# Kernel tuning notes

Measured on AMD Instinct MI355X. Metric: run time of the kernel, lower is better.

## Reference

```python
import jax, jax.numpy as jnp
import numpy as np
from jax import lax


def _nextpow2(v):
    return int(np.ceil(np.log2(abs(v))))


def _dct_matrix(N):
    # Orthonormal DCT-II matrix C: dct(x, norm='ortho') along last axis == x @ C.T
    # C is orthogonal, so idct(y, norm='ortho') == y @ C.
    n = jnp.arange(N, dtype=jnp.float32)
    k = n[:, None]
    C = 2.0 * jnp.cos(jnp.pi * (2.0 * n[None, :] + 1.0) * k / (2.0 * N))
    s = jnp.where(jnp.arange(N) == 0,
                  1.0 / jnp.sqrt(4.0 * N),
                  1.0 / jnp.sqrt(2.0 * N)).astype(jnp.float32)
    return s[:, None] * C


def setup_inputs() -> dict:
    key = jax.random.key(0)
    x = jax.random.normal(key, (2, 1, 128, 128), dtype=jnp.float32)
    tau = jnp.asarray(7.7e-11, dtype=jnp.float32)
    chi = jnp.asarray(0.03, dtype=jnp.float32)
    return {"x": x, "tau": tau, "chi": chi}


def _forward(x, c0=1.0, sigma=1.0):
    B, _, Nz, Nx = x.shape
    Lx = 2 ** (_nextpow2(2 * Nx) + 1)  # padded width (512 for Nx=128)
    Ly = 2 ** (_nextpow2(2 * Nz) + 1)  # padded height (512 for Nz=128)
    Cy = _dct_matrix(Ly)
    Cx = Cy if Lx == Ly else _dct_matrix(Lx)

    # np.block([[Z, W, ZP_col], [Z, Z, ZP_col], [ZP_row]]) places W at rows 0:Nz, cols Nx:2Nx
    P = jnp.zeros((B, Ly, Lx), x.dtype).at[:, 0:Nz, Nx:2 * Nx].set(x[:, 0])

    # 2D orthonormal DCT-II: P_hat = Cy @ P @ Cx.T
    P_hat = jnp.einsum('ki,bij,lj->bkl', Cy, P, Cx)

    # Only row 0 of the 2D IDCT is kept per timestep; row-0 of the axis-0 IDCT is
    # a fixed weighted sum with weights a[k] = Cy[k, 0].
    a = Cy[:, 0]
    M = a[None, :, None] * P_hat  # (B, Ly, Lx)

    kx = jnp.arange(Lx, dtype=jnp.float32) / Lx * jnp.pi
    ky = jnp.arange(Ly, dtype=jnp.float32) / Ly * jnp.pi
    F = jnp.sqrt(ky[:, None] ** 2 + kx[None, :] ** 2)  # f.T in the source: (Ly, Lx)

    def step(carry, t):
        phase = jnp.cos(c0 * F * t)                 # (Ly, Lx), shared over batch
        return carry, jnp.einsum('kj,bkj->bj', phase, M)

    _, V = lax.scan(step, None, jnp.arange(Ly, dtype=jnp.float32))  # (T, B, Lx)

    # Remaining IDCT along the last axis, then /3
    Pdet = jnp.transpose(V @ Cx, (1, 0, 2)) / 3.0   # (B, T=Ly, Lx)

    # additive noise: N(0, sigma * std(Pdet)) per batch element (np.std -> ddof=0)
    std = jnp.std(Pdet, axis=(1, 2), keepdims=True)
    noise = jax.random.normal(jax.random.key(42), Pdet.shape, Pdet.dtype) * (sigma * std)
    return (Pdet + noise)[:, None]                  # (B, 1, Ly, Lx)


def reference(x, tau, chi):
    # tau, chi are module parameters but unused in the original forward path
    return _forward(x)
```

## Files before the change

### kernel.cpp

```cpp
#include <hip/hip_runtime.h>
#include <stdint.h>
#include <math.h>


#define HALF_N 262144
#define PI_F 3.14159274101257324f


__device__ __forceinline__ uint32_t rotl32(uint32_t v, int r) {
  return (v << r) | (v >> (32 - r));
}

__device__ __forceinline__ float erfinv_xla(float x) {
  float w = -log1pf(__fmul_rn(-x, x));
  float p;
  if (w < 5.0f) {
    w = w - 2.5f;
    p = 2.81022636e-08f;
    p = fmaf(p, w, 3.43273939e-07f);
    p = fmaf(p, w, -3.5233877e-06f);
    p = fmaf(p, w, -4.39150654e-06f);
    p = fmaf(p, w, 0.00021858087f);
    p = fmaf(p, w, -0.00125372503f);
    p = fmaf(p, w, -0.00417768164f);
    p = fmaf(p, w, 0.246640727f);
    p = fmaf(p, w, 1.50140941f);
  } else {
    w = __fsqrt_rn(w) - 3.0f;
    p = -0.000200214257f;
    p = fmaf(p, w, 0.000100950558f);
    p = fmaf(p, w, 0.00134934322f);
    p = fmaf(p, w, -0.00367342844f);
    p = fmaf(p, w, 0.00573950773f);
    p = fmaf(p, w, -0.0076224613f);
    p = fmaf(p, w, 0.00943887047f);
    p = fmaf(p, w, 1.00167406f);
    p = fmaf(p, w, 2.83297682f);
  }
  return p * x;
}

__device__ __forceinline__ float cy_elem(float n2p1, float kf, float sc) {
  float t1 = __fmul_rn(PI_F, n2p1);
  float arg = __fmul_rn(t1, kf) * (1.0f / 1024.0f);
  return __fmul_rn(sc, __fmul_rn(2.0f, __cosf(arg)));
}

__global__ __launch_bounds__(512, 4) void stageB_kernel(const float* __restrict__ x,
                                                        float* __restrict__ Vt) {
  __shared__ float cyl[128];
  __shared__ float us[256];
  __shared__ float fs[512];
  __shared__ float msf[1024];
  int j = blockIdx.x;
  int tid = threadIdx.x;
  float jf = (float)j;
  if (tid < 128) {
    float scj = (j == 0) ? (1.0f / __fsqrt_rn(2048.0f)) : 0.03125f;
    cyl[tid] = cy_elem((float)(2 * (128 + tid) + 1), jf, scj);
  }
  __syncthreads();
  if (tid < 256) {
    int b = tid >> 7, i = tid & 127;
    const float* xr = x + (b * 128 + i) * 128;
    float accA = 0.0f, accB = 0.0f;
    for (int jj = 0; jj < 128; jj += 8) {
      float4 xa = *(const float4*)&xr[jj];
      float4 xb = *(const float4*)&xr[jj + 4];
      float4 ca = *(const float4*)&cyl[jj];
      float4 cb = *(const float4*)&cyl[jj + 4];
      accA = fmaf(xa.x, ca.x, accA); accB = fmaf(xa.y, ca.y, accB);
      accA = fmaf(xa.z, ca.z, accA); accB = fmaf(xa.w, ca.w, accB);
      accA = fmaf(xb.x, cb.x, accA); accB = fmaf(xb.y, cb.y, accB);
      accA = fmaf(xb.z, cb.z, accA); accB = fmaf(xb.w, cb.w, accB);
    }
    us[tid] = accA + accB;
  }
  __syncthreads();
  {
    float kf = (float)tid;
    float sc = (tid == 0) ? (1.0f / __fsqrt_rn(2048.0f)) : 0.03125f;
    float a = cy_elem(1.0f, kf, sc);
    float acc0 = __fmul_rn(a, us[0]);
    float acc1 = __fmul_rn(a, us[128]);
    float accA0 = 0.f, accA1 = 0.f;
    {
      float c1 = cy_elem(3.0f, kf, sc);
      float c2 = cy_elem(5.0f, kf, sc);
      float c3 = cy_elem(7.0f, kf, sc);
      acc0 = fmaf(c1, us[1], acc0);   acc1 = fmaf(c1, us[129], acc1);
      accA0 = fmaf(c2, us[2], accA0); accA1 = fmaf(c2, us[130], accA1);
      acc0 = fmaf(c3, us[3], acc0);   acc1 = fmaf(c3, us[131], acc1);
    }
    for (int i = 4; i < 128; i += 4) {
      float b0 = (float)(2 * i + 1);
      float c0 = cy_elem(b0, kf, sc);
      float c1 = cy_elem(__fadd_rn(b0, 2.0f), kf, sc);
      float c2 = cy_elem(__fadd_rn(b0, 4.0f), kf, sc);
      float c3 = cy_elem(__fadd_rn(b0, 6.0f), kf, sc);
      float4 u0 = *(const float4*)&us[i];
      float4 u1 = *(const float4*)&us[128 + i];
      acc0 = fmaf(c0, u0.x, acc0);   acc1 = fmaf(c0, u1.x, acc1);
      accA0 = fmaf(c1, u0.y, accA0); accA1 = fmaf(c1, u1.y, accA1);
      acc0 = fmaf(c2, u0.z, acc0);   acc1 = fmaf(c2, u1.z, acc1);
      accA0 = fmaf(c3, u0.w, accA0); accA1 = fmaf(c3, u1.w, accA1);
    }
    acc0 += accA0;
    acc1 += accA1;
    const float w0 = PI_F / 512.0f;
    float ky = __fmul_rn(kf, w0);
    float kx = __fmul_rn(jf, w0);
    fs[tid] = __fsqrt_rn(__fadd_rn(__fmul_rn(ky, ky), __fmul_rn(kx, kx)));
    msf[2 * tid] = __fmul_rn(a, acc0);
    msf[2 * tid + 1] = __fmul_rn(a, acc1);
  }
  __syncthreads();
  float tf = (float)tid;
  float acc0 = 0.f, acc1 = 0.f, acc2 = 0.f, acc3 = 0.f;
  for (int k0 = 0; k0 < 512; k0 += 8) {
    float4 f0 = *(const float4*)&fs[k0];
    float4 f1 = *(const float4*)&fs[k0 + 4];
    float4 m0 = *(const float4*)&msf[2 * k0];
    float4 m1 = *(const float4*)&msf[2 * k0 + 4];
    float4 m2 = *(const float4*)&msf[2 * k0 + 8];
    float4 m3 = *(const float4*)&msf[2 * k0 + 12];
    float ph0 = __cosf(__fmul_rn(f0.x, tf));
    float ph1 = __cosf(__fmul_rn(f0.y, tf));
    float ph2 = __cosf(__fmul_rn(f0.z, tf));
    float ph3 = __cosf(__fmul_rn(f0.w, tf));
    float ph4 = __cosf(__fmul_rn(f1.x, tf));
    float ph5 = __cosf(__fmul_rn(f1.y, tf));
    float ph6 = __cosf(__fmul_rn(f1.z, tf));
    float ph7 = __cosf(__fmul_rn(f1.w, tf));
    acc0 = fmaf(ph0, m0.x, acc0); acc1 = fmaf(ph0, m0.y, acc1);
    acc2 = fmaf(ph1, m0.z, acc2); acc3 = fmaf(ph1, m0.w, acc3);
    acc0 = fmaf(ph2, m1.x, acc0); acc1 = fmaf(ph2, m1.y, acc1);
    acc2 = fmaf(ph3, m1.z, acc2); acc3 = fmaf(ph3, m1.w, acc3);
    acc0 = fmaf(ph4, m2.x, acc0); acc1 = fmaf(ph4, m2.y, acc1);
    acc2 = fmaf(ph5, m2.z, acc2); acc3 = fmaf(ph5, m2.w, acc3);
    acc0 = fmaf(ph6, m3.x, acc0); acc1 = fmaf(ph6, m3.y, acc1);
    acc2 = fmaf(ph7, m3.z, acc2); acc3 = fmaf(ph7, m3.w, acc3);
  }
  Vt[(j << 10) + tid] = acc0 + acc2;
  Vt[(j << 10) + 512 + tid] = acc1 + acc3;
}

__global__ __launch_bounds__(256, 4) void stageC_kernel(const float* __restrict__ Vt,
                                                        float* __restrict__ out,
                                                        float* __restrict__ partial) {
  __shared__ float vq[2048];
  int tpair = blockIdx.x >> 1;
  int lhalf = blockIdx.x & 1;
  int t0 = tpair << 1;
  int tid = threadIdx.x;
#pragma unroll
  for (int r = 0; r < 2; ++r) {
    int j = tid + (r << 8);
    const float* base = Vt + (j << 10);
    vq[(j << 2) + 0] = base[t0];
    vq[(j << 2) + 1] = base[512 + t0];
    vq[(j << 2) + 2] = base[t0 + 1];
    vq[(j << 2) + 3] = base[512 + t0 + 1];
  }
  __syncthreads();
  int l = (lhalf << 8) + tid;
  float t1 = __fmul_rn(PI_F, (float)(2 * l + 1));
  float cth = __cosf(__fmul_rn(t1, 1.0f) * (1.0f / 1024.0f));
  float k2 = cth + cth;
  float cy0 = __fmul_rn(1.0f / __fsqrt_rn(2048.0f), 2.0f);
  float c16 = __fmul_rn(cy0, 16.0f);
  float4 v0 = *(const float4*)&vq[0];
  float a00 = __fmul_rn(c16, v0.x);
  float a01 = __fmul_rn(c16, v0.y);
  float a10 = __fmul_rn(c16, v0.z);
  float a11 = __fmul_rn(c16, v0.w);
  float c_m1, c_m2;
  {
    float4 v1 = *(const float4*)&vq[1 << 2];
    a00 = fmaf(cth, v1.x, a00); a01 = fmaf(cth, v1.y, a01);
    a10 = fmaf(cth, v1.z, a10); a11 = fmaf(cth, v1.w, a11);
    float c2v = __cosf(__fmul_rn(t1, 2.0f) * (1.0f / 1024.0f));
    float4 v2 = *(const float4*)&vq[2 << 2];
    a00 = fmaf(c2v, v2.x, a00); a01 = fmaf(c2v, v2.y, a01);
    a10 = fmaf(c2v, v2.z, a10); a11 = fmaf(c2v, v2.w, a11);
    c_m2 = cth; c_m1 = c2v;
#pragma unroll
    for (int j = 3; j < 16; ++j) {
      float cn = fmaf(k2, c_m1, -c_m2);
      float4 v = *(const float4*)&vq[j << 2];
      a00 = fmaf(cn, v.x, a00); a01 = fmaf(cn, v.y, a01);
      a10 = fmaf(cn, v.z, a10); a11 = fmaf(cn, v.w, a11);
      c_m2 = c_m1; c_m1 = cn;
    }
  }
  for (int j0 = 16; j0 < 512; j0 += 16) {
    float jb = (float)j0;
    float ca = __cosf(__fmul_rn(t1, jb) * (1.0f / 1024.0f));
    float cb = __cosf(__fmul_rn(t1, __fadd_rn(jb, 1.0f)) * (1.0f / 1024.0f));
    float4 va = *(const float4*)&vq[j0 << 2];
    a00 = fmaf(ca, va.x, a00); a01 = fmaf(ca, va.y, a01);
    a10 = fmaf(ca, va.z, a10); a11 = fmaf(ca, va.w, a11);
    float4 vb = *(const float4*)&vq[(j0 + 1) << 2];
    a00 = fmaf(cb, vb.x, a00); a01 = fmaf(cb, vb.y, a01);
    a10 = fmaf(cb, vb.z, a10); a11 = fmaf(cb, vb.w, a11);
    c_m2 = ca; c_m1 = cb;
#pragma unroll
    for (int n = 2; n < 16; ++n) {
      float cn = fmaf(k2, c_m1, -c_m2);
      float4 v = *(const float4*)&vq[(j0 + n) << 2];
      a00 = fmaf(cn, v.x, a00); a01 = fmaf(cn, v.y, a01);
      a10 = fmaf(cn, v.z, a10); a11 = fmaf(cn, v.w, a11);
      c_m2 = c_m1; c_m1 = cn;
    }
  }
  float p00 = __fmul_rn(a00, 0.0625f) / 3.0f;
  float p01 = __fmul_rn(a01, 0.0625f) / 3.0f;
  float p10 = __fmul_rn(a10, 0.0625f) / 3.0f;
  float p11 = __fmul_rn(a11, 0.0625f) / 3.0f;
  out[(t0 << 9) + l] = p00;
  out[((t0 + 1) << 9) + l] = p10;
  out[HALF_N + (t0 << 9) + l] = p01;
  out[HALF_N + ((t0 + 1) << 9) + l] = p11;
  float s0 = p00 + p10, q0 = fmaf(p00, p00, p10 * p10);
  float s1 = p01 + p11, q1 = fmaf(p01, p01, p11 * p11);
  for (int off = 32; off > 0; off >>= 1) {
    s0 += __shfl_down(s0, off);
    q0 += __shfl_down(q0, off);
    s1 += __shfl_down(s1, off);
    q1 += __shfl_down(q1, off);
  }
  __shared__ float red[4][4];
  int wave = tid >> 6;
  if ((tid & 63) == 0) {
    red[wave][0] = s0; red[wave][1] = q0; red[wave][2] = s1; red[wave][3] = q1;
  }
  __syncthreads();
  if (tid == 0) {
    float a0 = 0.f, a1 = 0.f, a2 = 0.f, a3 = 0.f;
    for (int wv = 0; wv < 4; ++wv) {
      a0 += red[wv][0]; a1 += red[wv][1]; a2 += red[wv][2]; a3 += red[wv][3];
    }
    partial[blockIdx.x * 4 + 0] = a0;
    partial[blockIdx.x * 4 + 1] = a1;
    partial[blockIdx.x * 4 + 2] = a2;
    partial[blockIdx.x * 4 + 3] = a3;
  }
}

__global__ __launch_bounds__(256) void noise_kernel(float* __restrict__ out,
                                                    const float* __restrict__ partial) {
  int tid = threadIdx.x;
  const float4* pq = (const float4*)partial;
  float4 pa = pq[tid];
  float4 pb = pq[tid + 256];
  float s0 = pa.x + pb.x, q0 = pa.y + pb.y, s1 = pa.z + pb.z, q1 = pa.w + pb.w;
  for (int off = 32; off > 0; off >>= 1) {
    s0 += __shfl_down(s0, off);
    q0 += __shfl_down(q0, off);
    s1 += __shfl_down(s1, off);
    q1 += __shfl_down(q1, off);
  }
  __shared__ float red[4][4];
  int wave = tid >> 6;
  if ((tid & 63) == 0) {
    red[wave][0] = s0; red[wave][1] = q0; red[wave][2] = s1; red[wave][3] = q1;
  }
  __syncthreads();
  float S = red[0][0] + red[1][0] + red[2][0] + red[3][0];
  float Q = red[0][1] + red[1][1] + red[2][1] + red[3][1];
  float S2 = red[0][2] + red[1][2] + red[2][2] + red[3][2];
  float Q2 = red[0][3] + red[1][3] + red[2][3] + red[3][3];
  const float invN = 1.0f / 262144.0f;
  float m0 = S * invN, m1 = S2 * invN;
  float std0 = __fsqrt_rn(fmaxf(Q * invN - m0 * m0, 0.0f));
  float std1 = __fsqrt_rn(fmaxf(Q2 * invN - m1 * m1, 0.0f));

  int i = blockIdx.x * 256 + tid;
  uint32_t x0 = 0u;
  uint32_t x1 = (uint32_t)i;
  const uint32_t k0 = 0u, k1 = 42u;
  const uint32_t k2 = k0 ^ k1 ^ 0x1BD11BDAu;
  x0 += k0; x1 += k1;
#define QR(r) x0 += x1; x1 = rotl32(x1, r); x1 ^= x0;
  QR(13) QR(15) QR(26) QR(6)
  x0 += k1; x1 += k2 + 1u;
  QR(17) QR(29) QR(16) QR(24)
  x0 += k2; x1 += k0 + 2u;
  QR(13) QR(15) QR(26) QR(6)
  x0 += k0; x1 += k1 + 3u;
  QR(17) QR(29) QR(16) QR(24)
  x0 += k1; x1 += k2 + 4u;
  QR(13) QR(15) QR(26) QR(6)
  x0 += k2; x1 += k0 + 5u;
#undef QR
  uint32_t bits = x0 ^ x1;
  const float lo = __uint_as_float(0xBF7FFFFFu);
  float f = __uint_as_float((bits >> 9) | 0x3F800000u) - 1.0f;
  float u = fmaxf(lo, __fadd_rn(__fmul_rn(f, 2.0f), lo));
  const float sqrt2 = 1.41421356237309515f;
  out[i] += (i < HALF_N ? std0 : std1) * (sqrt2 * erfinv_xla(u));
}

extern "C" void kernel_launch(void* const* d_in, const int* in_sizes, int n_in,
                              void* d_out, int out_size, void* d_ws, size_t ws_size,
                              hipStream_t stream) {
  const float* x = (const float*)d_in[0];
  float* ws = (float*)d_ws;
  float* Vt      = ws;
  float* partial = ws + 524288;
  float* out = (float*)d_out;

  stageB_kernel<<<512, 512, 0, stream>>>(x, Vt);
  stageC_kernel<<<512, 256, 0, stream>>>(Vt, out, partial);
  noise_kernel<<<2048, 256, 0, stream>>>(out, partial);
}
```

Measured before the change: 118.5 us.

## Replace per-timestep cosine evaluations with Chebyshev recurrence and k-split reduction

```diff
diff --git a/kernel.cpp b/kernel.cpp
--- a/kernel.cpp
+++ b/kernel.cpp
@@ -50,8 +50,8 @@
                                                         float* __restrict__ Vt) {
   __shared__ float cyl[128];
   __shared__ float us[256];
-  __shared__ float fs[512];
-  __shared__ float msf[1024];
+  __shared__ float4 kq[512];
+  __shared__ float red[8][512];
   int j = blockIdx.x;
   int tid = threadIdx.x;
   float jf = (float)j;
@@ -110,39 +110,48 @@
     const float w0 = PI_F / 512.0f;
     float ky = __fmul_rn(kf, w0);
     float kx = __fmul_rn(jf, w0);
-    fs[tid] = __fsqrt_rn(__fadd_rn(__fmul_rn(ky, ky), __fmul_rn(kx, kx)));
-    msf[2 * tid] = __fmul_rn(a, acc0);
-    msf[2 * tid + 1] = __fmul_rn(a, acc1);
-  }
-  __syncthreads();
-  float tf = (float)tid;
-  float acc0 = 0.f, acc1 = 0.f, acc2 = 0.f, acc3 = 0.f;
-  for (int k0 = 0; k0 < 512; k0 += 8) {
-    float4 f0 = *(const float4*)&fs[k0];
-    float4 f1 = *(const float4*)&fs[k0 + 4];
-    float4 m0 = *(const float4*)&msf[2 * k0];
-    float4 m1 = *(const float4*)&msf[2 * k0 + 4];
-    float4 m2 = *(const float4*)&msf[2 * k0 + 8];
-    float4 m3 = *(const float4*)&msf[2 * k0 + 12];
-    float ph0 = __cosf(__fmul_rn(f0.x, tf));
-    float ph1 = __cosf(__fmul_rn(f0.y, tf));
-    float ph2 = __cosf(__fmul_rn(f0.z, tf));
-    float ph3 = __cosf(__fmul_rn(f0.w, tf));
-    float ph4 = __cosf(__fmul_rn(f1.x, tf));
-    float ph5 = __cosf(__fmul_rn(f1.y, tf));
-    float ph6 = __cosf(__fmul_rn(f1.z, tf));
-    float ph7 = __cosf(__fmul_rn(f1.w, tf));
-    acc0 = fmaf(ph0, m0.x, acc0); acc1 = fmaf(ph0, m0.y, acc1);
-    acc2 = fmaf(ph1, m0.z, acc2); acc3 = fmaf(ph1, m0.w, acc3);
-    acc0 = fmaf(ph2, m1.x, acc0); acc1 = fmaf(ph2, m1.y, acc1);
-    acc2 = fmaf(ph3, m1.z, acc2); acc3 = fmaf(ph3, m1.w, acc3);
-    acc0 = fmaf(ph4, m2.x, acc0); acc1 = fmaf(ph4, m2.y, acc1);
-    acc2 = fmaf(ph5, m2.z, acc2); acc3 = fmaf(ph5, m2.w, acc3);
-    acc0 = fmaf(ph6, m3.x, acc0); acc1 = fmaf(ph6, m3.y, acc1);
-    acc2 = fmaf(ph7, m3.z, acc2); acc3 = fmaf(ph7, m3.w, acc3);
-  }
-  Vt[(j << 10) + tid] = acc0 + acc2;
-  Vt[(j << 10) + 512 + tid] = acc1 + acc3;
+    float fsv = __fsqrt_rn(__fadd_rn(__fmul_rn(ky, ky), __fmul_rn(kx, kx)));
+    kq[tid] = make_float4(fsv, __fmul_rn(a, acc0), __fmul_rn(a, acc1), 0.0f);
+  }
+  __syncthreads();
+  int kg = tid >> 6, tg = tid & 63;
+  int kbeg = kg << 6;
+  float tfa = (float)tg;
+  float tfb = (float)(tg + 64);
+  float a0[8], a1[8];
+#pragma unroll
+  for (int n = 0; n < 8; ++n) { a0[n] = 0.0f; a1[n] = 0.0f; }
+  for (int kk = 0; kk < 64; ++kk) {
+    float4 q = kq[kbeg + kk];
+    float F = q.x, m0 = q.y, m1 = q.z;
+    float cs = __cosf(__fmul_rn(F, 64.0f));
+    float k2 = cs + cs;
+    float ca = __cosf(__fmul_rn(F, tfa));
+    float cb = __cosf(__fmul_rn(F, tfb));
+    a0[0] = fmaf(ca, m0, a0[0]); a1[0] = fmaf(ca, m1, a1[0]);
+    a0[1] = fmaf(cb, m0, a0[1]); a1[1] = fmaf(cb, m1, a1[1]);
+#pragma unroll
+    for (int n = 2; n < 8; ++n) {
+      float cn = fmaf(k2, cb, -ca);
+      a0[n] = fmaf(cn, m0, a0[n]); a1[n] = fmaf(cn, m1, a1[n]);
+      ca = cb; cb = cn;
+    }
+  }
+#pragma unroll
+  for (int n = 0; n < 8; ++n) red[kg][(n << 6) + tg] = a0[n];
+  __syncthreads();
+  float s0 = red[0][tid];
+#pragma unroll
+  for (int g = 1; g < 8; ++g) s0 += red[g][tid];
+  __syncthreads();
+#pragma unroll
+  for (int n = 0; n < 8; ++n) red[kg][(n << 6) + tg] = a1[n];
+  __syncthreads();
+  float s1 = red[0][tid];
+#pragma unroll
+  for (int g = 1; g < 8; ++g) s1 += red[g][tid];
+  Vt[(j << 10) + tid] = s0;
+  Vt[(j << 10) + 512 + tid] = s1;
 }
 
 __global__ __launch_bounds__(256, 4) void stageC_kernel(const float* __restrict__ Vt,
```

New measurement: 110.9 us. -6.4%, faster.
